# Kernel optimization log

Hardware: AMD Instinct MI355X
Metric: run time of the kernel (lower is better)

The kernel has to match this reference:

```python
import jax, jax.numpy as jnp
import numpy as np

EMBED_DIM = 384
NUM_HEADS = 6
EPS = 1e-5

def _conv_proj(x, w_dw, gamma, beta, mean, var, stride):
    # x: [B,H,W,C]; depthwise 3x3 conv (groups=C), pad 1, then BN (inference), then flatten HW.
    C = x.shape[-1]
    y = jax.lax.conv_general_dilated(
        x, w_dw, window_strides=(stride, stride), padding=[(1, 1), (1, 1)],
        dimension_numbers=("NHWC", "HWIO", "NHWC"), feature_group_count=C)
    y = (y - mean) * jax.lax.rsqrt(var + EPS) * gamma + beta
    B, H, W, Cc = y.shape
    return y.reshape(B, H * W, Cc)

def _heads(x):
    # [B, L, C] -> [B, nH, L, hd]
    B, L, C = x.shape
    hd = C // NUM_HEADS
    return x.reshape(B, L, NUM_HEADS, hd).transpose(0, 2, 1, 3)

def setup_inputs() -> dict:
    key = jax.random.key(0)
    ks = jax.random.split(key, 20)
    B, H, W, C = 64, 28, 28, EMBED_DIM
    inp = {
        "hidden_state": jax.random.normal(ks[0], (B, 1 + H * W, C), dtype=jnp.float32),
        "height": H,
        "width": W,
    }
    std = 0.02
    for i, p in enumerate(("q", "k", "v")):
        inp[f"w_dw_{p}"] = jax.random.normal(ks[1 + i], (3, 3, 1, C), dtype=jnp.float32) * std
        inp[f"bn_gamma_{p}"] = jnp.ones((C,), jnp.float32) + 0.1 * jax.random.normal(ks[4 + i], (C,))
        inp[f"bn_beta_{p}"] = 0.1 * jax.random.normal(ks[7 + i], (C,))
        inp[f"bn_mean_{p}"] = 0.1 * jax.random.normal(ks[10 + i], (C,))
        inp[f"bn_var_{p}"] = jnp.ones((C,), jnp.float32) + 0.1 * jax.random.uniform(ks[13 + i], (C,))
        inp[f"W_{p}"] = jax.random.normal(ks[16 + i], (C, C), dtype=jnp.float32) * std
        inp[f"b_{p}"] = jnp.zeros((C,), jnp.float32)
    return inp

def reference(hidden_state, height, width,
              w_dw_q, bn_gamma_q, bn_beta_q, bn_mean_q, bn_var_q, W_q, b_q,
              w_dw_k, bn_gamma_k, bn_beta_k, bn_mean_k, bn_var_k, W_k, b_k,
              w_dw_v, bn_gamma_v, bn_beta_v, bn_mean_v, bn_var_v, W_v, b_v):
    B, _, C = hidden_state.shape
    scale = C ** (-0.5)  # note: embed_dim**-0.5, as in the source
    cls_token = hidden_state[:, :1]
    x = hidden_state[:, 1:].reshape(B, height, width, C)

    q = _conv_proj(x, w_dw_q, bn_gamma_q, bn_beta_q, bn_mean_q, bn_var_q, stride=1)
    k = _conv_proj(x, w_dw_k, bn_gamma_k, bn_beta_k, bn_mean_k, bn_var_k, stride=2)
    v = _conv_proj(x, w_dw_v, bn_gamma_v, bn_beta_v, bn_mean_v, bn_var_v, stride=2)

    q = jnp.concatenate((cls_token, q), axis=1)
    k = jnp.concatenate((cls_token, k), axis=1)
    v = jnp.concatenate((cls_token, v), axis=1)

    q = _heads(q @ W_q + b_q)  # [B,h,Lq,d]
    k = _heads(k @ W_k + b_k)  # [B,h,Lk,d]
    v = _heads(v @ W_v + b_v)

    scores = jnp.einsum("bhqd,bhkd->bhqk", q, k) * scale
    probs = jax.nn.softmax(scores, axis=-1)
    ctx = jnp.einsum("bhqk,bhkd->bhqd", probs, v)
    Lq = ctx.shape[2]
    return ctx.transpose(0, 2, 1, 3).reshape(B, Lq, C)
```

## Files before the change

kernel.cpp:

```cpp
#include <hip/hip_runtime.h>
#include <hip/hip_bf16.h>

#define C_DIM 384
#define BATCH 64
#define LQ 785
#define LK 197
#define NHEADS 6
#define HDIM 64
#define QTILES 785
#define KTILES 197

typedef __hip_bfloat16 bf16;
typedef __attribute__((ext_vector_type(8))) short short8;
typedef __attribute__((ext_vector_type(4))) float float4v;

__device__ __forceinline__ float bf2f(bf16 x) { return __bfloat162float(x); }
__device__ __forceinline__ bf16 f2bf(float x) { return __float2bfloat16(x); }
__device__ __forceinline__ float lo16f(unsigned int u) { return __uint_as_float(u << 16); }
__device__ __forceinline__ float hi16f(unsigned int u) { return __uint_as_float(u & 0xffff0000u); }
__device__ __forceinline__ unsigned short bfb(float x) {
    union { bf16 h; unsigned short s; } u; u.h = f2bf(x); return u.s;
}
__device__ __forceinline__ unsigned int pk2(float a, float b) {
    return ((unsigned int)bfb(b) << 16) | bfb(a);
}

template<bool F32>
__device__ __forceinline__ float ldx(const void* p, size_t i) {
    if constexpr (F32) return ((const float*)p)[i];
    else return bf2f(((const bf16*)p)[i]);
}
template<bool F32>
__device__ __forceinline__ void stx(void* p, size_t i, float v) {
    if constexpr (F32) ((float*)p)[i] = v;
    else ((bf16*)p)[i] = f2bf(v);
}
template<bool F32>
__device__ __forceinline__ void ld4(const void* p, size_t i, float* o) {
    if constexpr (F32) {
        float4 v = *(const float4*)((const float*)p + i);
        o[0] = v.x; o[1] = v.y; o[2] = v.z; o[3] = v.w;
    } else {
        uint2 u = *(const uint2*)((const bf16*)p + i);
        o[0] = lo16f(u.x); o[1] = hi16f(u.x); o[2] = lo16f(u.y); o[3] = hi16f(u.y);
    }
}
template<bool F32>
__device__ __forceinline__ void ld2(const void* p, size_t i, float* o) {
    if constexpr (F32) {
        float2 v = *(const float2*)((const float*)p + i);
        o[0] = v.x; o[1] = v.y;
    } else {
        unsigned int u = *(const unsigned int*)((const bf16*)p + i);
        o[0] = lo16f(u); o[1] = hi16f(u);
    }
}

__global__ void detect_kernel(const void* varq, int* flag) {
    const unsigned short* u = (const unsigned short*)varq;
    int votes = 0;
    #pragma unroll
    for (int i = 0; i < 4; ++i) {
        float b = __uint_as_float(((unsigned int)u[2 * i]) << 16);
        votes += (b > 0.5f && b < 2.0f) ? 1 : 0;
    }
    *flag = (votes == 4) ? 1 : 0;
}

template<bool F32>
__global__ __launch_bounds__(256) void repack_kernel(const int* __restrict__ flagp,
    const void* __restrict__ W0, const void* __restrict__ W1, const void* __restrict__ W2,
    bf16* __restrict__ dst)
{
    if (*flagp != (F32 ? 0 : 1)) return;
    const void* W = blockIdx.y == 0 ? W0 : (blockIdx.y == 1 ? W1 : W2);
    bf16* d = dst + (size_t)blockIdx.y * (C_DIM * C_DIM);
    int idx = blockIdx.x * 256 + threadIdx.x;
    int k = idx / C_DIM, nc = idx - k * C_DIM;
    int nt = nc >> 4, n = nc & 15, kt = k >> 5, q = (k >> 3) & 3, j = k & 7;
    d[(size_t)((((nt * 12 + kt) * 4 + q) * 16 + n) * 8 + j)] = f2bf(ldx<F32>(W, idx));
}

template<bool F32>
__device__ __forceinline__ void foldw(const void* __restrict__ wdw,
    const void* __restrict__ gamma, const void* __restrict__ beta,
    const void* __restrict__ mean,  const void* __restrict__ var,
    int c0, float w[9][2], float sh[2])
{
    float g[2], be[2], mu[2], vv[2];
    ld2<F32>(gamma, c0, g); ld2<F32>(beta, c0, be);
    ld2<F32>(mean,  c0, mu); ld2<F32>(var,  c0, vv);
    float sc[2];
    #pragma unroll
    for (int i = 0; i < 2; ++i) {
        sc[i] = g[i] * rsqrtf(vv[i] + 1e-5f);
        sh[i] = be[i] - mu[i] * sc[i];
    }
    #pragma unroll
    for (int p = 0; p < 9; ++p) {
        float t[2];
        ld2<F32>(wdw, (size_t)p * C_DIM + c0, t);
        w[p][0] = t[0] * sc[0];
        w[p][1] = t[1] * sc[1];
    }
}

template<int OJH, bool F32>
__device__ __forceinline__ void conv_quad(int b, int oik, int c2,
    const void* __restrict__ hs,
    const void* wq_, const void* gq, const void* beq, const void* muq, const void* vaq,
    const void* wk_, const void* gk, const void* bek, const void* muk, const void* vak,
    const void* wv_, const void* gv, const void* bev, const void* muv, const void* vav,
    bf16* __restrict__ qa, bf16* __restrict__ ka, bf16* __restrict__ va)
{
    int c0 = c2 * 2;
    float wq[9][2], wk[9][2], wv[9][2], shq[2], shk[2], shv[2];
    foldw<F32>(wq_, gq, beq, muq, vaq, c0, wq, shq);
    foldw<F32>(wk_, gk, bek, muk, vak, c0, wk, shk);
    foldw<F32>(wv_, gv, bev, muv, vav, c0, wv, shv);

    size_t hb = (size_t)b * (LQ * C_DIM);
    int i0 = 2 * oik - 1;
    bool rv[4];
    #pragma unroll
    for (int ri = 0; ri < 4; ++ri) rv[ri] = ((unsigned)(i0 + ri)) < 28u;

    float xw[4][3][2];
    constexpr int JJ0 = 14 * OJH - 1;

    int rq0 = b * LQ + 1 + 2 * oik * 28;
    int rq1 = rq0 + 28;
    int rk  = b * LK + 1 + oik * 14;

    #pragma unroll
    for (int s = 0; s < 16; ++s) {
        const int jj = JJ0 + s;
        const int sl = ((jj % 3) + 3) % 3;
        const bool cval = (jj >= 0) && (jj < 28);
        #pragma unroll
        for (int ri = 0; ri < 4; ++ri) {
            if (cval && rv[ri])
                ld2<F32>(hs, hb + (size_t)(1 + (i0 + ri) * 28 + jj) * C_DIM + c0, xw[ri][sl]);
            else { xw[ri][sl][0] = 0.f; xw[ri][sl][1] = 0.f; }
        }
        if (s >= 2) {
            const int jc = jj - 1;
            float a0[2] = {}, a1[2] = {};
            #pragma unroll
            for (int di = 0; di < 3; ++di)
                #pragma unroll
                for (int dj = 0; dj < 3; ++dj) {
                    const int s2 = (((jc - 1 + dj) % 3) + 3) % 3;
                    const int t = di * 3 + dj;
                    a0[0] = fmaf(xw[di][s2][0],     wq[t][0], a0[0]);
                    a0[1] = fmaf(xw[di][s2][1],     wq[t][1], a0[1]);
                    a1[0] = fmaf(xw[di + 1][s2][0], wq[t][0], a1[0]);
                    a1[1] = fmaf(xw[di + 1][s2][1], wq[t][1], a1[1]);
                }
            *(unsigned int*)&qa[(size_t)(rq0 + jc) * C_DIM + c0] = pk2(a0[0] + shq[0], a0[1] + shq[1]);
            *(unsigned int*)&qa[(size_t)(rq1 + jc) * C_DIM + c0] = pk2(a1[0] + shq[0], a1[1] + shq[1]);
            if ((jc & 1) == 0) {
                float k0[2] = {}, v0[2] = {};
                #pragma unroll
                for (int di = 0; di < 3; ++di)
                    #pragma unroll
                    for (int dj = 0; dj < 3; ++dj) {
                        const int s2 = (((jc - 1 + dj) % 3) + 3) % 3;
                        const int t = di * 3 + dj;
                        k0[0] = fmaf(xw[di][s2][0], wk[t][0], k0[0]);
                        k0[1] = fmaf(xw[di][s2][1], wk[t][1], k0[1]);
                        v0[0] = fmaf(xw[di][s2][0], wv[t][0], v0[0]);
                        v0[1] = fmaf(xw[di][s2][1], wv[t][1], v0[1]);
                    }
                int ro = rk + (jc >> 1);
                *(unsigned int*)&ka[(size_t)ro * C_DIM + c0] = pk2(k0[0] + shk[0], k0[1] + shk[1]);
                *(unsigned int*)&va[(size_t)ro * C_DIM + c0] = pk2(v0[0] + shv[0], v0[1] + shv[1]);
            }
        }
    }
}

#define CONV4_BLOCKS 960
template<bool F32>
__global__ __launch_bounds__(384) void conv4_kernel(
    const int* __restrict__ flagp, const void* __restrict__ hs,
    const void* wq, const void* gq, const void* beq, const void* muq, const void* vaq,
    const void* wk, const void* gk, const void* bek, const void* muk, const void* vak,
    const void* wv, const void* gv, const void* bev, const void* muv, const void* vav,
    bf16* __restrict__ qa, bf16* __restrict__ ka, bf16* __restrict__ va)
{
    if (*flagp != (F32 ? 0 : 1)) return;
    int bid = blockIdx.x;
    int tid = threadIdx.x;
    if (bid < 896) {
        int w = (bid & 7) * 112 + (bid >> 3);
        int b = w / 14, oik = w - b * 14;
        int c2 = tid % 192, ojh = tid / 192;
        if (ojh == 0)
            conv_quad<0, F32>(b, oik, c2, hs, wq, gq, beq, muq, vaq,
                              wk, gk, bek, muk, vak, wv, gv, bev, muv, vav, qa, ka, va);
        else
            conv_quad<1, F32>(b, oik, c2, hs, wq, gq, beq, muq, vaq,
                              wk, gk, bek, muk, vak, wv, gv, bev, muv, vav, qa, ka, va);
    } else {
        int b = bid - 896;
        if (tid < 192) {
            int c0 = tid * 2;
            float v2[2];
            ld2<F32>(hs, (size_t)b * (LQ * C_DIM) + c0, v2);
            unsigned int pk = pk2(v2[0], v2[1]);
            *(unsigned int*)&qa[(size_t)(b * LQ) * C_DIM + c0] = pk;
            *(unsigned int*)&ka[(size_t)(b * LK) * C_DIM + c0] = pk;
            *(unsigned int*)&va[(size_t)(b * LK) * C_DIM + c0] = pk;
        }
    }
}

template<bool F32>
__global__ __launch_bounds__(256) void gemm_frag_kernel(
    const int* __restrict__ flagp,
    const bf16* __restrict__ qa, const bf16* __restrict__ ka, const bf16* __restrict__ va,
    const bf16* __restrict__ wrep,
    const void* __restrict__ b_q, const void* __restrict__ b_k, const void* __restrict__ b_v,
    void* __restrict__ outq, bf16* __restrict__ kbuf, bf16* __restrict__ vbuf)
{
    if (*flagp != (F32 ? 0 : 1)) return;

    int bidx = blockIdx.x;
    const bf16* A; const bf16* wr; const void* bias; int tile, mode;
    if (bidx < QTILES)                { mode = 0; tile = bidx;                  A = qa; wr = wrep;                          bias = b_q; }
    else if (bidx < QTILES + KTILES)  { mode = 1; tile = bidx - QTILES;         A = ka; wr = wrep + (size_t)C_DIM * C_DIM;     bias = b_k; }
    else                              { mode = 2; tile = bidx - QTILES - KTILES; A = va; wr = wrep + (size_t)2 * C_DIM * C_DIM; bias = b_v; }

    const bf16* Abase = A + (size_t)tile * (64 * C_DIM);
    const short8* wf = (const short8*)wr;
    int tid = threadIdx.x;
    int lane = tid & 63, wave = tid >> 6;
    int mrow = lane & 15, quad = lane >> 4;
    float4v acc[4][6] = {};

    for (int kt = 0; kt < 12; ++kt) {
        short8 a[4];
        #pragma unroll
        for (int mt = 0; mt < 4; ++mt)
            a[mt] = *(const short8*)(Abase + (size_t)(mt * 16 + mrow) * C_DIM + (kt * 4 + quad) * 8);
        #pragma unroll
        for (int nt = 0; nt < 6; ++nt) {
            short8 bfrag = wf[(size_t)((wave * 6 + nt) * 12 + kt) * 64 + lane];
            #pragma unroll
            for (int mt = 0; mt < 4; ++mt)
                acc[mt][nt] = __builtin_amdgcn_mfma_f32_16x16x32_bf16(a[mt], bfrag, acc[mt][nt], 0, 0, 0);
        }
    }

    #pragma unroll
    for (int nt = 0; nt < 6; ++nt) {
        int col = wave * 96 + nt * 16 + mrow;
        float bb = ldx<F32>(bias, col);
        #pragma unroll
        for (int mt = 0; mt < 4; ++mt) {
            int row = tile * 64 + mt * 16 + quad * 4;
            #pragma unroll
            for (int r2 = 0; r2 < 4; ++r2) {
                float v = acc[mt][nt][r2] + bb;
                size_t o = (size_t)(row + r2) * C_DIM + col;
                if (mode == 0)      stx<F32>(outq, o, v);
                else if (mode == 1) kbuf[o] = f2bf(v);
                else                vbuf[o] = f2bf(v);
            }
        }
    }
}

template<int L, int OW, int STRIDE, bool F32, bool OF32>
__global__ __launch_bounds__(256) void fused_proj_kernel(
    const int* __restrict__ flagp,
    const void* __restrict__ hs, const void* __restrict__ wdw,
    const void* __restrict__ gamma, const void* __restrict__ beta,
    const void* __restrict__ mean,  const void* __restrict__ var,
    const bf16* __restrict__ Wrep,  const void* __restrict__ bias,
    void* __restrict__ O)
{
    if (*flagp != (F32 ? 0 : 1)) return;

    __shared__ bf16 A_s[64 * C_DIM];
    __shared__ float sc[C_DIM];
    __shared__ float sh[C_DIM];
    int tid = threadIdx.x;
    int m0 = blockIdx.x * 64;

    for (int c = tid; c < C_DIM; c += 256) {
        float s = ldx<F32>(gamma, c) * rsqrtf(ldx<F32>(var, c) + 1e-5f);
        sc[c] = s;
        sh[c] = ldx<F32>(beta, c) - ldx<F32>(mean, c) * s;
    }
    __syncthreads();

    for (int e = tid; e < 64 * 96; e += 256) {
        int m = e / 96;
        int c = (e - m * 96) * 4;
        int r = m0 + m;
        int b = r / L;
        int l = r - b * L;
        size_t hb = (size_t)b * (LQ * C_DIM);
        float v[4];
        if (l == 0) {
            ld4<F32>(hs, hb + c, v);
        } else {
            int p = l - 1;
            int oi = p / OW;
            int oj = p - oi * OW;
            float a0 = 0.f, a1 = 0.f, a2 = 0.f, a3 = 0.f;
            #pragma unroll
            for (int di = 0; di < 3; ++di) {
                int ii = oi * STRIDE - 1 + di;
                if (ii < 0 || ii >= 28) continue;
                #pragma unroll
                for (int dj = 0; dj < 3; ++dj) {
                    int jj = oj * STRIDE - 1 + dj;
                    if (jj < 0 || jj >= 28) continue;
                    float x[4], w[4];
                    ld4<F32>(hs, hb + (size_t)(1 + ii * 28 + jj) * C_DIM + c, x);
                    ld4<F32>(wdw, (size_t)(di * 3 + dj) * C_DIM + c, w);
                    a0 = fmaf(x[0], w[0], a0); a1 = fmaf(x[1], w[1], a1);
                    a2 = fmaf(x[2], w[2], a2); a3 = fmaf(x[3], w[3], a3);
                }
            }
            v[0] = a0 * sc[c + 0] + sh[c + 0];
            v[1] = a1 * sc[c + 1] + sh[c + 1];
            v[2] = a2 * sc[c + 2] + sh[c + 2];
            v[3] = a3 * sc[c + 3] + sh[c + 3];
        }
        int kt = c >> 5, q = (c >> 3) & 3, j = c & 7;
        int ofs = ((kt * 4 + q) * 64 + m) * 8 + j;
        ushort4 st = { bfb(v[0]), bfb(v[1]), bfb(v[2]), bfb(v[3]) };
        *(ushort4*)&A_s[ofs] = st;
    }
    __syncthreads();

    int lane = tid & 63, wave = tid >> 6;
    int mrow = lane & 15, quad = lane >> 4;
    float4v acc[4][6] = {};
    const short8* as = (const short8*)A_s;
    const short8* wr = (const short8*)Wrep;

    for (int kt = 0; kt < 12; ++kt) {
        short8 a[4];
        #pragma unroll
        for (int mt = 0; mt < 4; ++mt)
            a[mt] = as[(kt * 4 + quad) * 64 + mt * 16 + mrow];
        #pragma unroll
        for (int nt = 0; nt < 6; ++nt) {
            int ntg = wave * 6 + nt;
            short8 bfrag = wr[(size_t)(ntg * 12 + kt) * 64 + lane];
            #pragma unroll
            for (int mt = 0; mt < 4; ++mt)
                acc[mt][nt] = __builtin_amdgcn_mfma_f32_16x16x32_bf16(a[mt], bfrag, acc[mt][nt], 0, 0, 0);
        }
    }

    #pragma unroll
    for (int nt = 0; nt < 6; ++nt) {
        int col = wave * 96 + nt * 16 + mrow;
        float bb = ldx<F32>(bias, col);
        #pragma unroll
        for (int mt = 0; mt < 4; ++mt) {
            int row = m0 + mt * 16 + quad * 4;
            #pragma unroll
            for (int r2 = 0; r2 < 4; ++r2)
                stx<OF32>(O, (size_t)(row + r2) * C_DIM + col, acc[mt][nt][r2] + bb);
        }
    }
}

template<bool F32>
__global__ __launch_bounds__(256) void attn_kernel(
    const int* __restrict__ flagp,
    const bf16* __restrict__ kg,
    const bf16* __restrict__ vg,
    void* __restrict__ qo)
{
    if (*flagp != (F32 ? 0 : 1)) return;

    __shared__ unsigned short Kf[8 * 2 * 64 * 8];
    __shared__ unsigned short Vf[4 * 4 * 64 * 8];
    __shared__ unsigned short Ps[4 * 16 * 136];

    int tid = threadIdx.x;
    int lane = tid & 63, wave = tid >> 6;
    int m = lane & 15, quad = lane >> 4;
    int bid = blockIdx.x;
    int qb = bid % 13;
    int bh = bid / 13;
    int h = bh % NHEADS, b = bh / NHEADS;
    int qbase = qb * 64 + wave * 16;

    int qrow = min(qbase + m, LQ - 1);
    size_t qoff = ((size_t)b * LQ + qrow) * C_DIM + h * HDIM;
    short8 aq[2];
    #pragma unroll
    for (int ks = 0; ks < 2; ++ks) {
        float t[8];
        ld4<F32>(qo, qoff + ks * 32 + quad * 8, t);
        ld4<F32>(qo, qoff + ks * 32 + quad * 8 + 4, t + 4);
        short8 f;
        #pragma unroll
        for (int j = 0; j < 8; ++j) f[j] = (short)bfb(t[j]);
        aq[ks] = f;
    }

    const float scale = 0.05103103630798287f;
    float4v ctx[4] = {};
    float lsum4[4] = {};
    size_t kvbase = (size_t)b * LK * C_DIM + h * HDIM;

    for (int c = 0; c < 2; ++c) {
        int c0 = c * 128;
        for (int e = tid; e < 1024; e += 256) {
            int col = e >> 3, d8 = e & 7;
            int gcol = c0 + col;
            uint4 val = {0, 0, 0, 0};
            if (gcol < LK) val = *(const uint4*)(kg + kvbase + (size_t)gcol * C_DIM + d8 * 8);
            int nt = col >> 4, n = col & 15, ks = d8 >> 2, q = d8 & 3;
            *(uint4*)&Kf[((nt * 2 + ks) * 64 + q * 16 + n) * 8] = val;
        }
        for (int e = tid; e < 1024; e += 256) {
            int p = e >> 3, d8 = e & 7;
            int gp = c0 + p;
            int ks = p >> 5, q = (p >> 3) & 3, j = p & 7;
            int ntv = d8 >> 1, nl0 = (d8 & 1) * 8;
            if (gp < LK) {
                union { uint4 u; unsigned short s[8]; } val;
                val.u = *(const uint4*)(vg + kvbase + (size_t)gp * C_DIM + d8 * 8);
                #pragma unroll
                for (int i = 0; i < 8; ++i)
                    Vf[((ntv * 4 + ks) * 64 + q * 16 + nl0 + i) * 8 + j] = val.s[i];
            } else {
                #pragma unroll
                for (int i = 0; i < 8; ++i)
                    Vf[((ntv * 4 + ks) * 64 + q * 16 + nl0 + i) * 8 + j] = 0;
            }
        }
        __syncthreads();

        const short8* kf = (const short8*)Kf;
        unsigned short* pw = Ps + wave * (16 * 136);
        int ntmax = (c == 0) ? 8 : 5;
        for (int nt = 0; nt < ntmax; ++nt) {
            float4v s = {0.f, 0.f, 0.f, 0.f};
            #pragma unroll
            for (int ks = 0; ks < 2; ++ks)
                s = __builtin_amdgcn_mfma_f32_16x16x32_bf16(aq[ks], kf[(nt * 2 + ks) * 64 + lane], s, 0, 0, 0);
            int coln = c0 + nt * 16 + m;
            bool valid = coln < LK;
            #pragma unroll
            for (int r = 0; r < 4; ++r) {
                float pv = valid ? __expf(s[r] * scale) : 0.f;
                lsum4[r] += pv;
                pw[(quad * 4 + r) * 136 + nt * 16 + m] = bfb(pv);
            }
        }
        if (c == 1) {
            #pragma unroll
            for (int nt = 5; nt < 8; ++nt)
                #pragma unroll
                for (int r = 0; r < 4; ++r)
                    pw[(quad * 4 + r) * 136 + nt * 16 + m] = 0;
        }

        const short8* vf = (const short8*)Vf;
        const short8* pf = (const short8*)Ps;
        #pragma unroll
        for (int ks = 0; ks < 4; ++ks) {
            short8 ap = pf[wave * 272 + m * 17 + ks * 4 + quad];
            #pragma unroll
            for (int ntv = 0; ntv < 4; ++ntv)
                ctx[ntv] = __builtin_amdgcn_mfma_f32_16x16x32_bf16(ap, vf[(ntv * 4 + ks) * 64 + lane], ctx[ntv], 0, 0, 0);
        }
        __syncthreads();
    }

    float inv[4];
    #pragma unroll
    for (int r = 0; r < 4; ++r) {
        float t = lsum4[r];
        t += __shfl_xor(t, 1);
        t += __shfl_xor(t, 2);
        t += __shfl_xor(t, 4);
        t += __shfl_xor(t, 8);
        inv[r] = 1.f / t;
    }
    #pragma unroll
    for (int ntv = 0; ntv < 4; ++ntv) {
        #pragma unroll
        for (int r = 0; r < 4; ++r) {
            int row = qbase + quad * 4 + r;
            if (row < LQ)
                stx<F32>(qo, ((size_t)b * LQ + row) * C_DIM + h * HDIM + ntv * 16 + m, ctx[ntv][r] * inv[r]);
        }
    }
}

extern "C" void kernel_launch(void* const* d_in, const int* in_sizes, int n_in,
                              void* d_out, int out_size, void* d_ws, size_t ws_size,
                              hipStream_t stream)
{
    const void* hs    = d_in[0];
    const void* wdw_q = d_in[3];
    const void* g_q   = d_in[4];
    const void* be_q  = d_in[5];
    const void* mu_q  = d_in[6];
    const void* va_q  = d_in[7];
    const void* W_q   = d_in[8];
    const void* b_q   = d_in[9];
    const void* wdw_k = d_in[10];
    const void* g_k   = d_in[11];
    const void* be_k  = d_in[12];
    const void* mu_k  = d_in[13];
    const void* va_k  = d_in[14];
    const void* W_k   = d_in[15];
    const void* b_k   = d_in[16];
    const void* wdw_v = d_in[17];
    const void* g_v   = d_in[18];
    const void* be_v  = d_in[19];
    const void* mu_v  = d_in[20];
    const void* va_v  = d_in[21];
    const void* W_v   = d_in[22];
    const void* b_v   = d_in[23];

    const size_t QA = (size_t)QTILES * 24576;
    const size_t KA = (size_t)KTILES * 24576;
    const size_t NEED_BIG = 16 + 2 * (3 * (size_t)C_DIM * C_DIM + QA + 4 * KA);

    int*  flag = (int*)d_ws;
    bf16* wrep = (bf16*)((char*)d_ws + 16);
    bf16* wrq  = wrep;
    bf16* wrk  = wrep + (size_t)C_DIM * C_DIM;
    bf16* wrv  = wrep + (size_t)2 * C_DIM * C_DIM;

    detect_kernel<<<1, 1, 0, stream>>>(va_q, flag);
    repack_kernel<false><<<dim3(576, 3), 256, 0, stream>>>(flag, W_q, W_k, W_v, wrep);
    repack_kernel<true ><<<dim3(576, 3), 256, 0, stream>>>(flag, W_q, W_k, W_v, wrep);

    if (ws_size >= NEED_BIG) {
        bf16* qa   = wrep + (size_t)3 * C_DIM * C_DIM;
        bf16* ka   = qa + QA;
        bf16* vaa  = ka + KA;
        bf16* kbuf = vaa + KA;
        bf16* vbuf = kbuf + KA;

        conv4_kernel<false><<<CONV4_BLOCKS, 384, 0, stream>>>(flag, hs,
            wdw_q, g_q, be_q, mu_q, va_q, wdw_k, g_k, be_k, mu_k, va_k,
            wdw_v, g_v, be_v, mu_v, va_v, qa, ka, vaa);
        conv4_kernel<true ><<<CONV4_BLOCKS, 384, 0, stream>>>(flag, hs,
            wdw_q, g_q, be_q, mu_q, va_q, wdw_k, g_k, be_k, mu_k, va_k,
            wdw_v, g_v, be_v, mu_v, va_v, qa, ka, vaa);

        gemm_frag_kernel<false><<<QTILES + 2 * KTILES, 256, 0, stream>>>(flag,
            qa, ka, vaa, wrep, b_q, b_k, b_v, d_out, kbuf, vbuf);
        gemm_frag_kernel<true ><<<QTILES + 2 * KTILES, 256, 0, stream>>>(flag,
            qa, ka, vaa, wrep, b_q, b_k, b_v, d_out, kbuf, vbuf);

        attn_kernel<false><<<384 * 13, 256, 0, stream>>>(flag, kbuf, vbuf, d_out);
        attn_kernel<true ><<<384 * 13, 256, 0, stream>>>(flag, kbuf, vbuf, d_out);
    } else {
        bf16* kbuf = wrep + (size_t)3 * C_DIM * C_DIM;
        bf16* vbuf = kbuf + (size_t)BATCH * LK * C_DIM;

        fused_proj_kernel<LQ, 28, 1, false, false><<<LQ, 256, 0, stream>>>(flag, hs, wdw_q, g_q, be_q, mu_q, va_q, wrq, b_q, d_out);
        fused_proj_kernel<LQ, 28, 1, true,  true ><<<LQ, 256, 0, stream>>>(flag, hs, wdw_q, g_q, be_q, mu_q, va_q, wrq, b_q, d_out);
        fused_proj_kernel<LK, 14, 2, false, false><<<LK, 256, 0, stream>>>(flag, hs, wdw_k, g_k, be_k, mu_k, va_k, wrk, b_k, kbuf);
        fused_proj_kernel<LK, 14, 2, true,  false><<<LK, 256, 0, stream>>>(flag, hs, wdw_k, g_k, be_k, mu_k, va_k, wrk, b_k, kbuf);
        fused_proj_kernel<LK, 14, 2, false, false><<<LK, 256, 0, stream>>>(flag, hs, wdw_v, g_v, be_v, mu_v, va_v, wrv, b_v, vbuf);
        fused_proj_kernel<LK, 14, 2, true,  false><<<LK, 256, 0, stream>>>(flag, hs, wdw_v, g_v, be_v, mu_v, va_v, wrv, b_v, vbuf);

        attn_kernel<false><<<384 * 13, 256, 0, stream>>>(flag, kbuf, vbuf, d_out);
        attn_kernel<true ><<<384 * 13, 256, 0, stream>>>(flag, kbuf, vbuf, d_out);
    }
}
```

Before: 385.1 us.

## Store V transposed and padded so attention loads V fragments directly

Result: slower. 402.3 us (+4.5%).

```diff
diff --git a/kernel.cpp b/kernel.cpp
--- a/kernel.cpp
+++ b/kernel.cpp
@@ -9,6 +9,7 @@
 #define HDIM 64
 #define QTILES 785
 #define KTILES 197
+#define KPAD 208
 
 typedef __hip_bfloat16 bf16;
 typedef __attribute__((ext_vector_type(8))) short short8;
@@ -79,6 +80,15 @@
     int k = idx / C_DIM, nc = idx - k * C_DIM;
     int nt = nc >> 4, n = nc & 15, kt = k >> 5, q = (k >> 3) & 3, j = k & 7;
     d[(size_t)((((nt * 12 + kt) * 4 + q) * 16 + n) * 8 + j)] = f2bf(ldx<F32>(W, idx));
+}
+
+__global__ __launch_bounds__(256) void vtail_zero_kernel(bf16* __restrict__ vt) {
+    int i = blockIdx.x * 256 + threadIdx.x;
+    if (i < BATCH * C_DIM * (KPAD - LK)) {
+        int rc = i / (KPAD - LK);
+        int kp = LK + (i - rc * (KPAD - LK));
+        vt[(size_t)rc * KPAD + kp] = f2bf(0.f);
+    }
 }
 
 template<bool F32>
@@ -222,7 +232,7 @@
     const bf16* __restrict__ qa, const bf16* __restrict__ ka, const bf16* __restrict__ va,
     const bf16* __restrict__ wrep,
     const void* __restrict__ b_q, const void* __restrict__ b_k, const void* __restrict__ b_v,
-    void* __restrict__ outq, bf16* __restrict__ kbuf, bf16* __restrict__ vbuf)
+    void* __restrict__ outq, bf16* __restrict__ kbuf, bf16* __restrict__ vbuf_t)
 {
     if (*flagp != (F32 ? 0 : 1)) return;
 
@@ -263,10 +273,16 @@
             #pragma unroll
             for (int r2 = 0; r2 < 4; ++r2) {
                 float v = acc[mt][nt][r2] + bb;
-                size_t o = (size_t)(row + r2) * C_DIM + col;
-                if (mode == 0)      stx<F32>(outq, o, v);
-                else if (mode == 1) kbuf[o] = f2bf(v);
-                else                vbuf[o] = f2bf(v);
+                int rr = row + r2;
+                if (mode == 0) {
+                    stx<F32>(outq, (size_t)rr * C_DIM + col, v);
+                } else if (mode == 1) {
+                    kbuf[(size_t)rr * C_DIM + col] = f2bf(v);
+                } else {
+                    int bb2 = rr / LK;
+                    int kpos = rr - bb2 * LK;
+                    vbuf_t[(size_t)(bb2 * C_DIM + col) * KPAD + kpos] = f2bf(v);
+                }
             }
         }
     }
@@ -369,6 +385,140 @@
             #pragma unroll
             for (int r2 = 0; r2 < 4; ++r2)
                 stx<OF32>(O, (size_t)(row + r2) * C_DIM + col, acc[mt][nt][r2] + bb);
+        }
+    }
+}
+
+template<bool F32>
+__global__ __launch_bounds__(256) void attn_vt_kernel(
+    const int* __restrict__ flagp,
+    const bf16* __restrict__ kg,
+    const bf16* __restrict__ vt_g,
+    void* __restrict__ qo)
+{
+    if (*flagp != (F32 ? 0 : 1)) return;
+
+    __shared__ unsigned short Kf[8 * 2 * 64 * 8];
+    __shared__ unsigned short Vt[64 * 128];
+    __shared__ unsigned short Ps[4 * 16 * 128];
+
+    int tid = threadIdx.x;
+    int lane = tid & 63, wave = tid >> 6;
+    int m = lane & 15, quad = lane >> 4;
+    int bid = blockIdx.x;
+    int qb = bid % 13;
+    int bh = bid / 13;
+    int h = bh % NHEADS, b = bh / NHEADS;
+    int qbase = qb * 64 + wave * 16;
+
+    int rev4m = ((m & 1) << 3) | ((m & 2) << 1) | ((m & 4) >> 1) | ((m & 8) >> 3);
+    int revr[4];
+    #pragma unroll
+    for (int r = 0; r < 4; ++r) {
+        int rr = quad * 4 + r;
+        revr[r] = ((rr & 1) << 3) | ((rr & 2) << 1) | ((rr & 4) >> 1) | ((rr & 8) >> 3);
+    }
+
+    int qrow = min(qbase + m, LQ - 1);
+    size_t qoff = ((size_t)b * LQ + qrow) * C_DIM + h * HDIM;
+    short8 aq[2];
+    #pragma unroll
+    for (int ks = 0; ks < 2; ++ks) {
+        float t[8];
+        ld4<F32>(qo, qoff + ks * 32 + quad * 8, t);
+        ld4<F32>(qo, qoff + ks * 32 + quad * 8 + 4, t + 4);
+        short8 f;
+        #pragma unroll
+        for (int j = 0; j < 8; ++j) f[j] = (short)bfb(t[j]);
+        aq[ks] = f;
+    }
+
+    const float scale = 0.05103103630798287f;
+    float4v ctx[4] = {};
+    float lsum4[4] = {};
+    size_t kvbase = (size_t)b * LK * C_DIM + h * HDIM;
+    size_t vtbase = (size_t)(b * C_DIM + h * HDIM) * KPAD;
+
+    for (int c = 0; c < 2; ++c) {
+        int c0 = c * 128;
+        for (int e = tid; e < 1024; e += 256) {
+            int col = e >> 3, d8 = e & 7;
+            int gcol = c0 + col;
+            uint4 val = {0, 0, 0, 0};
+            if (gcol < LK) val = *(const uint4*)(kg + kvbase + (size_t)gcol * C_DIM + d8 * 8);
+            int nt = col >> 4, n = col & 15, ks = d8 >> 2, q = d8 & 3;
+            *(uint4*)&Kf[((nt * 2 + ks) * 64 + q * 16 + n) * 8] = val;
+        }
+        for (int e = tid; e < 1024; e += 256) {
+            int d = e >> 4, kc = e & 15;
+            uint4 val = {0, 0, 0, 0};
+            if (c0 + kc * 8 < KPAD)
+                val = *(const uint4*)(vt_g + vtbase + (size_t)d * KPAD + c0 + kc * 8);
+            *(uint4*)&Vt[(d << 7) + ((kc ^ (d & 15)) << 3)] = val;
+        }
+        __syncthreads();
+
+        const short8* kf = (const short8*)Kf;
+        unsigned short* pw = Ps + wave * (16 * 128);
+        int ntmax = (c == 0) ? 8 : 5;
+        for (int nt = 0; nt < ntmax; ++nt) {
+            float4v s = {0.f, 0.f, 0.f, 0.f};
+            #pragma unroll
+            for (int ks = 0; ks < 2; ++ks)
+                s = __builtin_amdgcn_mfma_f32_16x16x32_bf16(aq[ks], kf[(nt * 2 + ks) * 64 + lane], s, 0, 0, 0);
+            int coln = c0 + nt * 16 + m;
+            bool valid = coln < LK;
+            int chb = nt * 2 + (m >> 3);
+            int sub = m & 7;
+            #pragma unroll
+            for (int r = 0; r < 4; ++r) {
+                float pv = valid ? __expf(s[r] * scale) : 0.f;
+                lsum4[r] += pv;
+                pw[(((quad * 4 + r)) << 7) + ((chb ^ revr[r]) << 3) + sub] = bfb(pv);
+            }
+        }
+        if (c == 1) {
+            int sub = m & 7;
+            #pragma unroll
+            for (int nt = 5; nt < 8; ++nt) {
+                int chb = nt * 2 + (m >> 3);
+                #pragma unroll
+                for (int r = 0; r < 4; ++r)
+                    pw[(((quad * 4 + r)) << 7) + ((chb ^ revr[r]) << 3) + sub] = 0;
+            }
+        }
+
+        const short8* vts = (const short8*)Vt;
+        const short8* pf = (const short8*)Ps;
+        #pragma unroll
+        for (int ks = 0; ks < 4; ++ks) {
+            short8 ap = pf[wave * 256 + (m << 4) + ((ks * 4 + quad) ^ rev4m)];
+            #pragma unroll
+            for (int ntv = 0; ntv < 4; ++ntv) {
+                short8 bf_ = vts[((ntv * 16 + m) << 4) + ((ks * 4 + quad) ^ m)];
+                ctx[ntv] = __builtin_amdgcn_mfma_f32_16x16x32_bf16(ap, bf_, ctx[ntv], 0, 0, 0);
+            }
+        }
+        __syncthreads();
+    }
+
+    float inv[4];
+    #pragma unroll
+    for (int r = 0; r < 4; ++r) {
+        float t = lsum4[r];
+        t += __shfl_xor(t, 1);
+        t += __shfl_xor(t, 2);
+        t += __shfl_xor(t, 4);
+        t += __shfl_xor(t, 8);
+        inv[r] = 1.f / t;
+    }
+    #pragma unroll
+    for (int ntv = 0; ntv < 4; ++ntv) {
+        #pragma unroll
+        for (int r = 0; r < 4; ++r) {
+            int row = qbase + quad * 4 + r;
+            if (row < LQ)
+                stx<F32>(qo, ((size_t)b * LQ + row) * C_DIM + h * HDIM + ntv * 16 + m, ctx[ntv][r] * inv[r]);
         }
     }
 }
@@ -530,7 +680,8 @@
 
     const size_t QA = (size_t)QTILES * 24576;
     const size_t KA = (size_t)KTILES * 24576;
-    const size_t NEED_BIG = 16 + 2 * (3 * (size_t)C_DIM * C_DIM + QA + 4 * KA);
+    const size_t VT = (size_t)BATCH * C_DIM * KPAD;
+    const size_t NEED_BIG = 16 + 2 * (3 * (size_t)C_DIM * C_DIM + QA + 3 * KA + VT);
 
     int*  flag = (int*)d_ws;
     bf16* wrep = (bf16*)((char*)d_ws + 16);
@@ -543,11 +694,13 @@
     repack_kernel<true ><<<dim3(576, 3), 256, 0, stream>>>(flag, W_q, W_k, W_v, wrep);
 
     if (ws_size >= NEED_BIG) {
-        bf16* qa   = wrep + (size_t)3 * C_DIM * C_DIM;
-        bf16* ka   = qa + QA;
-        bf16* vaa  = ka + KA;
-        bf16* kbuf = vaa + KA;
-        bf16* vbuf = kbuf + KA;
+        bf16* qa    = wrep + (size_t)3 * C_DIM * C_DIM;
+        bf16* ka    = qa + QA;
+        bf16* vaa   = ka + KA;
+        bf16* kbuf  = vaa + KA;
+        bf16* vbuft = kbuf + KA;
+
+        vtail_zero_kernel<<<(BATCH * C_DIM * (KPAD - LK) + 255) / 256, 256, 0, stream>>>(vbuft);
 
         conv4_kernel<false><<<CONV4_BLOCKS, 384, 0, stream>>>(flag, hs,
             wdw_q, g_q, be_q, mu_q, va_q, wdw_k, g_k, be_k, mu_k, va_k,
@@ -557,12 +710,12 @@
             wdw_v, g_v, be_v, mu_v, va_v, qa, ka, vaa);
 
         gemm_frag_kernel<false><<<QTILES + 2 * KTILES, 256, 0, stream>>>(flag,
-            qa, ka, vaa, wrep, b_q, b_k, b_v, d_out, kbuf, vbuf);
+            qa, ka, vaa, wrep, b_q, b_k, b_v, d_out, kbuf, vbuft);
         gemm_frag_kernel<true ><<<QTILES + 2 * KTILES, 256, 0, stream>>>(flag,
-            qa, ka, vaa, wrep, b_q, b_k, b_v, d_out, kbuf, vbuf);
-
-        attn_kernel<false><<<384 * 13, 256, 0, stream>>>(flag, kbuf, vbuf, d_out);
-        attn_kernel<true ><<<384 * 13, 256, 0, stream>>>(flag, kbuf, vbuf, d_out);
+            qa, ka, vaa, wrep, b_q, b_k, b_v, d_out, kbuf, vbuft);
+
+        attn_vt_kernel<false><<<384 * 13, 256, 0, stream>>>(flag, kbuf, vbuft, d_out);
+        attn_vt_kernel<true ><<<384 * 13, 256, 0, stream>>>(flag, kbuf, vbuft, d_out);
     } else {
         bf16* kbuf = wrep + (size_t)3 * C_DIM * C_DIM;
         bf16* vbuf = kbuf + (size_t)BATCH * LK * C_DIM;
```
